# Kernel tuning notes

Measured on AMD Instinct MI355X. Metric: run time of the kernel, lower is better.

## Reference

```python
import jax, jax.numpy as jnp
import numpy as np

N, E, F, H, G = 50000, 1600000, 128, 128, 64
EPS = 1e-5  # BatchNorm eps


def setup_inputs() -> dict:
    key = jax.random.key(0)
    ks = jax.random.split(key, 16)
    x = jax.random.normal(ks[0], (N, F), dtype=jnp.float32)
    edge_index = jax.random.randint(ks[1], (2, E), 0, N, dtype=jnp.int64)
    batch = jnp.sort(jax.random.randint(ks[2], (N,), 0, G, dtype=jnp.int64))
    inp = {
        'x': x, 'edge_index': edge_index, 'batch': batch,
        'W1': jax.random.normal(ks[3], (F, H), dtype=jnp.float32) / np.sqrt(F),
        'b1': jnp.zeros((H,), jnp.float32),
        'bn1_gamma': jax.random.uniform(ks[4], (H,), jnp.float32, 0.5, 1.5),
        'bn1_beta': jax.random.normal(ks[5], (H,), jnp.float32) * 0.1,
        'bn1_mean': jax.random.normal(ks[6], (H,), jnp.float32) * 0.1,
        'bn1_var': jax.random.uniform(ks[7], (H,), jnp.float32, 0.5, 1.5),
        'W2': jax.random.normal(ks[8], (H, H), dtype=jnp.float32) / np.sqrt(H),
        'b2': jnp.zeros((H,), jnp.float32),
        'bn2_gamma': jax.random.uniform(ks[9], (H,), jnp.float32, 0.5, 1.5),
        'bn2_beta': jax.random.normal(ks[10], (H,), jnp.float32) * 0.1,
        'bn2_mean': jax.random.normal(ks[11], (H,), jnp.float32) * 0.1,
        'bn2_var': jax.random.uniform(ks[12], (H,), jnp.float32, 0.5, 1.5),
        'att_w': jax.random.normal(ks[13], (H, 1), dtype=jnp.float32) / np.sqrt(H),
        'cls_w': jax.random.normal(ks[14], (1, H), dtype=jnp.float32) / np.sqrt(H),
        'cls_b': jnp.zeros((1,), jnp.float32),
    }
    return inp


def gcn_conv(h, W, b, src, dst, n):
    # PyG GCNConv: linear, add self-loops, symmetric D^{-1/2}(A+I)D^{-1/2} aggregation, bias.
    hw = h @ W                                   # [n, H]
    loops = jnp.arange(n, dtype=src.dtype)
    s = jnp.concatenate([src, loops])
    d = jnp.concatenate([dst, loops])
    deg = jax.ops.segment_sum(jnp.ones_like(d, dtype=hw.dtype), d, num_segments=n)
    dis = jnp.where(deg > 0, jax.lax.rsqrt(deg), 0.0)
    norm = dis[s] * dis[d]                       # [E+n]
    msgs = hw[s] * norm[:, None]                 # gather + scale (memory-bound)
    return jax.ops.segment_sum(msgs, d, num_segments=n) + b


def batch_norm(h, gamma, beta, mean, var):
    return (h - mean) * gamma * jax.lax.rsqrt(var + EPS) + beta


def reference(x, edge_index, batch, W1, b1, bn1_gamma, bn1_beta, bn1_mean, bn1_var,
              W2, b2, bn2_gamma, bn2_beta, bn2_mean, bn2_var, att_w, cls_w, cls_b):
    n = x.shape[0]
    src, dst = edge_index[0], edge_index[1]
    # eval mode: dropout and edge-dropout are no-ops; BN uses running stats
    h = gcn_conv(x, W1, b1, src, dst, n)
    h = jax.nn.relu(batch_norm(h, bn1_gamma, bn1_beta, bn1_mean, bn1_var))
    h = gcn_conv(h, W2, b2, src, dst, n)
    h = jax.nn.relu(batch_norm(h, bn2_gamma, bn2_beta, bn2_mean, bn2_var))
    att = jax.nn.sigmoid(h @ att_w)              # [n, 1]
    g = jax.ops.segment_sum(h * att, batch, num_segments=G)  # [G, H]
    logits = g @ cls_w.T + cls_b                 # [G, 1]
    return logits, att
```

## Files before the change

### kernel.cpp

```cpp
#include <hip/hip_runtime.h>
#include <math.h>

#define NN 50000
#define HID 128
#define NG 64
#define BN_EPS 1e-5f

typedef __attribute__((ext_vector_type(8))) short short8;
typedef __attribute__((ext_vector_type(4))) float f32x4;

__device__ inline unsigned pack_bf2(float a, float b) {
    union { float f; unsigned u; } ua, ub;
    ua.f = a; ub.f = b;
    unsigned x = ua.u, y = ub.u;
    x += 0x7fffu + ((x >> 16) & 1u);
    y += 0x7fffu + ((y >> 16) & 1u);
    return (x >> 16) | (y & 0xffff0000u);
}
__device__ inline unsigned short bf16_1(float x) {
    union { float f; unsigned u; } v;
    v.f = x;
    unsigned r = v.u + 0x7fffu + ((v.u >> 16) & 1u);
    return (unsigned short)(r >> 16);
}
__device__ inline float2 unpack_bf2(unsigned v) {
    union { unsigned u; float f; } a, b;
    a.u = v << 16;
    b.u = v & 0xffff0000u;
    return make_float2(a.f, b.f);
}

#define NBKT 256
#define ETILE 4096
#define EPT   (ETILE / 256)
#define CAP   10240
#define ASTR 136

__global__ __launch_bounds__(128) void k_prep0(const float* __restrict__ W1,
                                               const float* __restrict__ W2,
                                               unsigned short* __restrict__ wt1,
                                               unsigned short* __restrict__ wt2,
                                               int* __restrict__ bcurP,
                                               const float* __restrict__ cls_b,
                                               float* __restrict__ logits) {
    int b = blockIdx.x;
    int t = threadIdx.x;
    if (b < 256) {
        int k = b & 127;
        const float* W = (b < 128) ? W1 : W2;
        unsigned short* wt = (b < 128) ? wt1 : wt2;
        wt[t * 128 + k] = bf16_1(W[k * 128 + t]);
    } else {
        #pragma unroll
        for (int i = 0; i < 32; ++i) bcurP[t * 32 + i] = 0;
        if (t < NG) logits[t] = cls_b[0];
    }
}

__device__ __forceinline__ void gemm1_tile(char* smem, int row0,
                                           const float* __restrict__ x,
                                           const unsigned short* __restrict__ wt1,
                                           unsigned short* __restrict__ zb,
                                           int n, int t) {
    typedef unsigned short ArowT[ASTR];
    ArowT* A = (ArowT*)smem;
    #pragma unroll
    for (int i = 0; i < 8; ++i) {
        int idx = t + i * 256;
        int r = idx >> 5;
        int c4 = (idx & 31) * 4;
        float4 v = make_float4(0.f, 0.f, 0.f, 0.f);
        if (row0 + r < n) v = *(const float4*)&x[(size_t)(row0 + r) * 128 + c4];
        uint2 p;
        p.x = pack_bf2(v.x, v.y);
        p.y = pack_bf2(v.z, v.w);
        *(uint2*)&A[r][c4] = p;
    }
    __syncthreads();
    int lane = t & 63;
    int wave = t >> 6;
    int m = lane & 15;
    int quad = lane >> 4;
    int r0 = wave * 16;
    short8 a[4];
    #pragma unroll
    for (int kt = 0; kt < 4; ++kt)
        a[kt] = *(const short8*)&A[r0 + m][kt * 32 + quad * 8];
    f32x4 acc[8];
    #pragma unroll
    for (int ct = 0; ct < 8; ++ct) acc[ct] = (f32x4){0.f, 0.f, 0.f, 0.f};
    short8 bcur[4], bnxt[4];
    {
        const unsigned short* wb = &wt1[(size_t)m * 128 + quad * 8];
        #pragma unroll
        for (int kt = 0; kt < 4; ++kt) bcur[kt] = *(const short8*)(wb + kt * 32);
    }
    #pragma unroll
    for (int ct = 0; ct < 8; ++ct) {
        if (ct < 7) {
            const unsigned short* wb = &wt1[(size_t)((ct + 1) * 16 + m) * 128 + quad * 8];
            #pragma unroll
            for (int kt = 0; kt < 4; ++kt) bnxt[kt] = *(const short8*)(wb + kt * 32);
        }
        #pragma unroll
        for (int kt = 0; kt < 4; ++kt)
            acc[ct] = __builtin_amdgcn_mfma_f32_16x16x32_bf16(a[kt], bcur[kt], acc[ct], 0, 0, 0);
        #pragma unroll
        for (int kt = 0; kt < 4; ++kt) bcur[kt] = bnxt[kt];
    }
    __syncthreads();
    #pragma unroll
    for (int ct = 0; ct < 8; ++ct) {
        int col = ct * 16 + m;
        #pragma unroll
        for (int reg = 0; reg < 4; ++reg)
            A[r0 + quad * 4 + reg][col] = bf16_1(acc[ct][reg]);
    }
    __syncthreads();
    #pragma unroll
    for (int i = 0; i < 4; ++i) {
        int idx = t + i * 256;
        int r = idx >> 4;
        int c8 = (idx & 15) * 8;
        int grow = row0 + r;
        if (grow < n)
            *(uint4*)&zb[(size_t)grow * 128 + c8] = *(const uint4*)&A[r][c8];
    }
}

struct SmemDist {
    int h[NBKT], sx[NBKT], cur[NBKT], gb[NBKT];
    unsigned stage[ETILE];
};

__global__ __launch_bounds__(256) void k_dist_gemm1(const int* __restrict__ src,
                                                    const int* __restrict__ dst,
                                                    int* __restrict__ bcurP,
                                                    unsigned* __restrict__ bpacked,
                                                    const float* __restrict__ x,
                                                    const unsigned short* __restrict__ wt1,
                                                    unsigned short* __restrict__ zb,
                                                    int E, int n, int DB) {
    __shared__ __align__(16) char smem[sizeof(SmemDist)];
    int t = threadIdx.x;
    int b = blockIdx.x;

    if (b >= DB) {
        gemm1_tile(smem, (b - DB) * 64, x, wt1, zb, n, t);
        return;
    }
    SmemDist* s = (SmemDist*)smem;
    s->h[t] = 0;
    __syncthreads();
    int base = b * ETILE;
    int dreg[EPT];
    #pragma unroll
    for (int i = 0; i < EPT; ++i) {
        int e = base + i * 256 + t;
        dreg[i] = (e < E) ? dst[e] : -1;
        if (dreg[i] >= 0) atomicAdd(&s->h[dreg[i] >> 8], 1);
    }
    __syncthreads();
    int c = s->h[t];
    s->sx[t] = c;
    __syncthreads();
    for (int off = 1; off < NBKT; off <<= 1) {
        int v = (t >= off) ? s->sx[t - off] : 0;
        __syncthreads();
        s->sx[t] += v;
        __syncthreads();
    }
    int nvalid = s->sx[NBKT - 1];
    int excl = s->sx[t] - c;
    __syncthreads();
    s->sx[t] = excl;
    s->cur[t] = excl;
    s->gb[t] = (c > 0) ? atomicAdd(&bcurP[t * 16], c) : 0;
    __syncthreads();
    #pragma unroll
    for (int i = 0; i < EPT; ++i) {
        int e = base + i * 256 + t;
        if (dreg[i] >= 0) {
            int d = dreg[i];
            int bkt = d >> 8;
            int p = atomicAdd(&s->cur[bkt], 1);
            s->stage[p] = ((unsigned)d << 16) | (unsigned)src[e];
        }
    }
    __syncthreads();
    for (int idx = t; idx < nvalid; idx += 256) {
        unsigned v = s->stage[idx];
        int bkt = (int)(v >> 24);
        int pos = s->gb[bkt] + (idx - s->sx[bkt]);
        bpacked[(size_t)bkt * CAP + pos] = v;
    }
}

struct SmemCSR {
    int cnt[NBKT], sA[NBKT], cur[NBKT];
    unsigned short stage[CAP];
};

__global__ __launch_bounds__(256) void k_csr_gemm1(const unsigned* __restrict__ bpacked,
                                                   const int* __restrict__ bcurP,
                                                   int* __restrict__ row_ptr,
                                                   int* __restrict__ degA,
                                                   float* __restrict__ dis,
                                                   unsigned short* __restrict__ col16,
                                                   const float* __restrict__ x,
                                                   const unsigned short* __restrict__ wt1,
                                                   unsigned short* __restrict__ zb,
                                                   int n, int NB, int row0B) {
    __shared__ __align__(16) char smem[sizeof(SmemCSR)];
    int t = threadIdx.x;
    int b = blockIdx.x;

    if (b >= NB) {
        gemm1_tile(smem, row0B + (b - NB) * 64, x, wt1, zb, n, t);
        return;
    }
    SmemCSR* s = (SmemCSR*)smem;
    int node0 = b << 8;
    int nn = n - node0;
    if (nn > 256) nn = 256;
    if (nn < 0) nn = 0;
    int e0 = b * CAP;
    int ne = bcurP[b * 16];
    s->cnt[t] = 0;
    __syncthreads();
    int n4 = (ne + 3) >> 2;
    for (int i = t; i < n4; i += 256) {
        uint4 v = *(const uint4*)&bpacked[e0 + 4 * i];
        int rem = ne - 4 * i;
        if (rem > 0) atomicAdd(&s->cnt[(v.x >> 16) & 255u], 1);
        if (rem > 1) atomicAdd(&s->cnt[(v.y >> 16) & 255u], 1);
        if (rem > 2) atomicAdd(&s->cnt[(v.z >> 16) & 255u], 1);
        if (rem > 3) atomicAdd(&s->cnt[(v.w >> 16) & 255u], 1);
    }
    __syncthreads();
    int c = s->cnt[t];
    s->sA[t] = c;
    __syncthreads();
    for (int off = 1; off < NBKT; off <<= 1) {
        int v = (t >= off) ? s->sA[t - off] : 0;
        __syncthreads();
        s->sA[t] += v;
        __syncthreads();
    }
    int excl = s->sA[t] - c;
    s->cur[t] = excl;
    if (t < nn) {
        row_ptr[node0 + t] = e0 + excl;
        degA[node0 + t] = c;
        dis[node0 + t] = rsqrtf((float)(c + 1));
    }
    __syncthreads();
    for (int i = t; i < n4; i += 256) {
        uint4 v = *(const uint4*)&bpacked[e0 + 4 * i];
        int rem = ne - 4 * i;
        unsigned vv[4] = {v.x, v.y, v.z, v.w};
        #pragma unroll
        for (int j = 0; j < 4; ++j) {
            if (rem > j) {
                int ld = (int)((vv[j] >> 16) & 255u);
                int p = atomicAdd(&s->cur[ld], 1);
                s->stage[p] = (unsigned short)(vv[j] & 0xFFFFu);
            }
        }
    }
    __syncthreads();
    int nw = (ne + 1) >> 1;
    for (int i = t; i < nw; i += 256) {
        unsigned w = (unsigned)s->stage[2 * i] | ((unsigned)s->stage[2 * i + 1] << 16);
        *(unsigned*)&col16[e0 + 2 * i] = w;
    }
}

__global__ __launch_bounds__(256) void k_scale(unsigned short* __restrict__ zb,
                                               const float* __restrict__ dis, int n) {
    int i = blockIdx.x * 256 + threadIdx.x;
    int r = i >> 4;
    if (r >= n) return;
    int c8 = (i & 15) * 8;
    float s = dis[r];
    uint4 v = *(const uint4*)&zb[(size_t)r * 128 + c8];
    unsigned* w = (unsigned*)&v;
    #pragma unroll
    for (int k = 0; k < 4; ++k) {
        float2 f = unpack_bf2(w[k]);
        w[k] = pack_bf2(f.x * s, f.y * s);
    }
    *(uint4*)&zb[(size_t)r * 128 + c8] = v;
}


__device__ __forceinline__ void gather_pipe(const unsigned short* __restrict__ hws,
                                            const unsigned short* __restrict__ col16,
                                            int e0, int deg, int md, int sl, int part,
                                            float* acc8) {
    int nt = (md + 7) >> 3;
    if (nt <= 0) return;
    int base = part << 4;
    uint4 vA[8], vB[8];
    int c0, c1, n0 = 0, n1 = 0;
    c0 = (sl < deg) ? (int)col16[e0 + sl] : 0;
    c1 = (sl + 16 < deg) ? (int)col16[e0 + 16 + sl] : 0;

    #pragma unroll
    for (int j = 0; j < 8; ++j) {
        int s = __shfl(c0, base + j);
        vA[j] = (j < deg) ? *(const uint4*)(hws + ((size_t)s << 7) + (sl << 3))
                          : make_uint4(0, 0, 0, 0);
    }
    int t = 0, ebase = 0;
    for (;;) {
        if (t + 4 < nt) {
            n0 = (ebase + 32 + sl < deg) ? (int)col16[e0 + ebase + 32 + sl] : 0;
            n1 = (ebase + 48 + sl < deg) ? (int)col16[e0 + ebase + 48 + sl] : 0;
        }
        if (t + 1 < nt) {
            int it0 = (t + 1) << 3;
            #pragma unroll
            for (int j = 0; j < 8; ++j) {
                int s = __shfl(c0, base + 8 + j);
                vB[j] = (it0 + j < deg) ? *(const uint4*)(hws + ((size_t)s << 7) + (sl << 3))
                                        : make_uint4(0, 0, 0, 0);
            }
        }
        #pragma unroll
        for (int j = 0; j < 8; ++j) {
            const unsigned* w = (const unsigned*)&vA[j];
            #pragma unroll
            for (int i2 = 0; i2 < 4; ++i2) {
                float2 f = unpack_bf2(w[i2]);
                acc8[2 * i2]     += f.x;
                acc8[2 * i2 + 1] += f.y;
            }
        }
        if (++t >= nt) break;
        if (t + 1 < nt) {
            int it0 = (t + 1) << 3;
            #pragma unroll
            for (int j = 0; j < 8; ++j) {
                int s = __shfl(c1, base + j);
                vA[j] = (it0 + j < deg) ? *(const uint4*)(hws + ((size_t)s << 7) + (sl << 3))
                                        : make_uint4(0, 0, 0, 0);
            }
        }
        #pragma unroll
        for (int j = 0; j < 8; ++j) {
            const unsigned* w = (const unsigned*)&vB[j];
            #pragma unroll
            for (int i2 = 0; i2 < 4; ++i2) {
                float2 f = unpack_bf2(w[i2]);
                acc8[2 * i2]     += f.x;
                acc8[2 * i2 + 1] += f.y;
            }
        }
        if (++t >= nt) break;
        if (t + 1 < nt) {
            int it0 = (t + 1) << 3;
            #pragma unroll
            for (int j = 0; j < 8; ++j) {
                int s = __shfl(c1, base + 8 + j);
                vB[j] = (it0 + j < deg) ? *(const uint4*)(hws + ((size_t)s << 7) + (sl << 3))
                                        : make_uint4(0, 0, 0, 0);
            }
        }
        #pragma unroll
        for (int j = 0; j < 8; ++j) {
            const unsigned* w = (const unsigned*)&vA[j];
            #pragma unroll
            for (int i2 = 0; i2 < 4; ++i2) {
                float2 f = unpack_bf2(w[i2]);
                acc8[2 * i2]     += f.x;
                acc8[2 * i2 + 1] += f.y;
            }
        }
        if (++t >= nt) break;
        if (t + 1 < nt) {
            int it0 = (t + 1) << 3;
            #pragma unroll
            for (int j = 0; j < 8; ++j) {
                int s = __shfl(n0, base + j);
                vA[j] = (it0 + j < deg) ? *(const uint4*)(hws + ((size_t)s << 7) + (sl << 3))
                                        : make_uint4(0, 0, 0, 0);
            }
        }
        #pragma unroll
        for (int j = 0; j < 8; ++j) {
            const unsigned* w = (const unsigned*)&vB[j];
            #pragma unroll
            for (int i2 = 0; i2 < 4; ++i2) {
                float2 f = unpack_bf2(w[i2]);
                acc8[2 * i2]     += f.x;
                acc8[2 * i2 + 1] += f.y;
            }
        }
        if (++t >= nt) break;
        c0 = n0; c1 = n1; ebase += 32;
    }
}


__global__ __launch_bounds__(256, 3) void k_agg1_gemm2(const unsigned short* __restrict__ zb,
                                                       const int* __restrict__ row_ptr,
                                                       const int* __restrict__ degA,
                                                       const unsigned short* __restrict__ col16,
                                                       const float* __restrict__ dis,
                                                       const float* __restrict__ bias,
                                                       const float* __restrict__ gamma,
                                                       const float* __restrict__ beta,
                                                       const float* __restrict__ mean,
                                                       const float* __restrict__ var,
                                                       const unsigned short* __restrict__ wt2,
                                                       unsigned short* __restrict__ hwsb2, int n) {
    __shared__ unsigned short H1[16][ASTR];
    __shared__ unsigned short C2[16][ASTR];
    int t = threadIdx.x;
    int wave = t >> 6, lane = t & 63;
    int sl = lane & 15, part = lane >> 4;
    int d = blockIdx.x * 16 + wave * 4 + part;
    bool active = (d < n);
    int e0 = 0, deg = 0;
    if (active) {
        e0 = row_ptr[d];
        deg = degA[d];
    }
    uint4 vs = make_uint4(0, 0, 0, 0);
    float dd = 0.f;
    if (active) {
        vs = *(const uint4*)(zb + ((size_t)d << 7) + (sl << 3));
        dd = dis[d];
    }
    int md = deg;
    md = max(md, __shfl_xor(md, 16));
    md = max(md, __shfl_xor(md, 32));

    float acc8[8] = {0, 0, 0, 0, 0, 0, 0, 0};
    gather_pipe(zb, col16, e0, deg, md, sl, part, acc8);

    unsigned outw[4] = {0, 0, 0, 0};
    if (active) {
        const unsigned* w = (const unsigned*)&vs;
        #pragma unroll
        for (int i2 = 0; i2 < 4; ++i2) {
            float2 f = unpack_bf2(w[i2]);
            acc8[2 * i2]     += f.x;
            acc8[2 * i2 + 1] += f.y;
        }
        int f0 = sl << 3;
        #pragma unroll
        for (int i2 = 0; i2 < 4; ++i2) {
            int f = f0 + 2 * i2;
            float2 bv = *(const float2*)&bias[f];
            float2 gm = *(const float2*)&gamma[f];
            float2 bt = *(const float2*)&beta[f];
            float2 mn = *(const float2*)&mean[f];
            float2 vr = *(const float2*)&var[f];
            float vx = acc8[2 * i2] * dd + bv.x;
            float vy = acc8[2 * i2 + 1] * dd + bv.y;
            float sx = gm.x * rsqrtf(vr.x + BN_EPS);
            float sy = gm.y * rsqrtf(vr.y + BN_EPS);
            float rx = fmaxf((vx - mn.x) * sx + bt.x, 0.f);
            float ry = fmaxf((vy - mn.y) * sy + bt.y, 0.f);
            outw[i2] = pack_bf2(rx, ry);
        }
    }
    int local = wave * 4 + part;
    *(uint4*)&H1[local][sl << 3] = *(uint4*)outw;
    __syncthreads();

    int m = sl;
    int quad = part;
    short8 a2[4];
    #pragma unroll
    for (int kt = 0; kt < 4; ++kt)
        a2[kt] = *(const short8*)&H1[m][kt * 32 + quad * 8];

    f32x4 acc2[2];
    acc2[0] = (f32x4){0.f, 0.f, 0.f, 0.f};
    acc2[1] = (f32x4){0.f, 0.f, 0.f, 0.f};
    #pragma unroll
    for (int i = 0; i < 2; ++i) {
        int ct = wave * 2 + i;
        const unsigned short* wb = &wt2[(size_t)(ct * 16 + m) * 128 + quad * 8];
        #pragma unroll
        for (int kt = 0; kt < 4; ++kt) {
            short8 b = *(const short8*)(wb + kt * 32);
            acc2[i] = __builtin_amdgcn_mfma_f32_16x16x32_bf16(a2[kt], b, acc2[i], 0, 0, 0);
        }
    }
    int gr = blockIdx.x * 16 + quad * 4;
    float ds2[4];
    #pragma unroll
    for (int reg = 0; reg < 4; ++reg)
        ds2[reg] = (gr + reg < n) ? dis[gr + reg] : 0.f;
    #pragma unroll
    for (int i = 0; i < 2; ++i) {
        int col = (wave * 2 + i) * 16 + m;
        #pragma unroll
        for (int reg = 0; reg < 4; ++reg)
            C2[quad * 4 + reg][col] = bf16_1(acc2[i][reg] * ds2[reg]);
    }
    __syncthreads();
    {
        int r = t >> 4;
        int c8 = (t & 15) * 8;
        int grow = blockIdx.x * 16 + r;
        if (grow < n)
            *(uint4*)&hwsb2[(size_t)grow * 128 + c8] = *(const uint4*)&C2[r][c8];
    }
}


__global__ __launch_bounds__(256, 3) void k_agg2_att_logit(const unsigned short* __restrict__ hwsb,
                                                           const int* __restrict__ row_ptr,
                                                           const int* __restrict__ degA,
                                                           const unsigned short* __restrict__ col16,
                                                           const float* __restrict__ dis,
                                                           const float* __restrict__ bias,
                                                           const float* __restrict__ gamma,
                                                           const float* __restrict__ beta,
                                                           const float* __restrict__ mean,
                                                           const float* __restrict__ var,
                                                           const int* __restrict__ batch,
                                                           const float* __restrict__ att_w,
                                                           const float* __restrict__ cls_w,
                                                           float* __restrict__ att_out,
                                                           float* __restrict__ logits, int n) {
    __shared__ int   sg[16];
    __shared__ float sv[16];
    int t = threadIdx.x;
    int wave = t >> 6, lane = t & 63;
    int sl = lane & 15, part = lane >> 4;
    int d = blockIdx.x * 16 + wave * 4 + part;
    bool active = (d < n);
    int e0 = 0, deg = 0;
    if (active) {
        e0 = row_ptr[d];
        deg = degA[d];
    }
    uint4 vs = make_uint4(0, 0, 0, 0);
    float dd = 0.f;
    int g = -1;
    if (active) {
        vs = *(const uint4*)(hwsb + ((size_t)d << 7) + (sl << 3));
        dd = dis[d];
        g = batch[d];
    }
    int md = deg;
    md = max(md, __shfl_xor(md, 16));
    md = max(md, __shfl_xor(md, 32));

    float acc8[8] = {0, 0, 0, 0, 0, 0, 0, 0};
    gather_pipe(hwsb, col16, e0, deg, md, sl, part, acc8);

    float contrib = 0.f;
    float p = 0.f, q = 0.f;
    if (active) {
        const unsigned* w = (const unsigned*)&vs;
        #pragma unroll
        for (int i2 = 0; i2 < 4; ++i2) {
            float2 f = unpack_bf2(w[i2]);
            acc8[2 * i2]     += f.x;
            acc8[2 * i2 + 1] += f.y;
        }
        int f0 = sl << 3;
        #pragma unroll
        for (int i2 = 0; i2 < 4; ++i2) {
            int f = f0 + 2 * i2;
            float2 bv = *(const float2*)&bias[f];
            float2 gm = *(const float2*)&gamma[f];
            float2 bt = *(const float2*)&beta[f];
            float2 mn = *(const float2*)&mean[f];
            float2 vr = *(const float2*)&var[f];
            float vx = acc8[2 * i2] * dd + bv.x;
            float vy = acc8[2 * i2 + 1] * dd + bv.y;
            float sx = gm.x * rsqrtf(vr.x + BN_EPS);
            float sy = gm.y * rsqrtf(vr.y + BN_EPS);
            float rx = fmaxf((vx - mn.x) * sx + bt.x, 0.f);
            float ry = fmaxf((vy - mn.y) * sy + bt.y, 0.f);
            float2 aw = *(const float2*)&att_w[f];
            float2 cw = *(const float2*)&cls_w[f];
            p += rx * aw.x + ry * aw.y;
            q += rx * cw.x + ry * cw.y;
        }
    }
    #pragma unroll
    for (int off = 1; off < 16; off <<= 1) {
        p += __shfl_xor(p, off);
        q += __shfl_xor(q, off);
    }
    if (active) {
        float a = 1.f / (1.f + expf(-p));
        if (sl == 0) att_out[d] = a;
        contrib = a * q;
    }
    if (sl == 0) {
        sg[wave * 4 + part] = g;
        sv[wave * 4 + part] = contrib;
    }
    __syncthreads();
    if (t == 0) {
        int cur = -1;
        float acc = 0.f;
        #pragma unroll
        for (int i = 0; i < 16; ++i) {
            int gi = sg[i];
            if (gi < 0) continue;
            if (gi != cur) {
                if (cur >= 0) atomicAdd(&logits[cur], acc);
                cur = gi;
                acc = 0.f;
            }
            acc += sv[i];
        }
        if (cur >= 0) atomicAdd(&logits[cur], acc);
    }
}


extern "C" void kernel_launch(void* const* d_in, const int* in_sizes, int n_in,
                              void* d_out, int out_size, void* d_ws, size_t ws_size,
                              hipStream_t stream) {
    const float* x   = (const float*)d_in[0];
    const int*   ei  = (const int*)d_in[1];
    const int*   bat = (const int*)d_in[2];
    const float* W1  = (const float*)d_in[3];
    const float* b1  = (const float*)d_in[4];
    const float* g1  = (const float*)d_in[5];
    const float* bt1 = (const float*)d_in[6];
    const float* mn1 = (const float*)d_in[7];
    const float* vr1 = (const float*)d_in[8];
    const float* W2  = (const float*)d_in[9];
    const float* b2  = (const float*)d_in[10];
    const float* g2  = (const float*)d_in[11];
    const float* bt2 = (const float*)d_in[12];
    const float* mn2 = (const float*)d_in[13];
    const float* vr2 = (const float*)d_in[14];
    const float* attw = (const float*)d_in[15];
    const float* clsw = (const float*)d_in[16];
    const float* clsb = (const float*)d_in[17];

    int E = in_sizes[1] / 2;
    int n = in_sizes[2];
    const int* src = ei;
    const int* dst = ei + E;
    int NB = (n + 255) >> 8;

    char* ws = (char*)d_ws;
    auto alloc = [&](size_t bytes) {
        void* p = (void*)ws;
        ws += (bytes + 255) & ~(size_t)255;
        return p;
    };
    int*            bcurP   = (int*)alloc(NBKT * 16 * 4);
    unsigned*       bpacked = (unsigned*)alloc((size_t)NBKT * CAP * 4);
    int*            row_ptr = (int*)alloc((size_t)n * 4);
    int*            degA    = (int*)alloc((size_t)n * 4);
    unsigned short* col16   = (unsigned short*)alloc(((size_t)NBKT * CAP + 1024) * 2);
    float*          dis     = (float*)alloc((size_t)n * 4);
    unsigned short* zb      = (unsigned short*)alloc((size_t)n * 128 * 2);
    unsigned short* hwsb2   = (unsigned short*)alloc((size_t)n * 128 * 2);
    unsigned short* wt1     = (unsigned short*)alloc(128 * 128 * 2);
    unsigned short* wt2     = (unsigned short*)alloc(128 * 128 * 2);

    float* out = (float*)d_out;
    int DB = (E + ETILE - 1) / ETILE;
    int gb = (n + 63) / 64;
    int G1A = gb / 2;
    int G1B = gb - G1A;
    int ab = (n + 15) / 16;
    int sb = (n * 16 + 255) / 256;

    k_prep0<<<257, 128, 0, stream>>>(W1, W2, wt1, wt2, bcurP, clsb, out);
    k_dist_gemm1<<<DB + G1A, 256, 0, stream>>>(src, dst, bcurP, bpacked, x, wt1, zb,
                                               E, n, DB);
    k_csr_gemm1<<<NB + G1B, 256, 0, stream>>>(bpacked, bcurP, row_ptr, degA, dis,
                                              col16, x, wt1, zb, n, NB, G1A * 64);
    k_scale<<<sb, 256, 0, stream>>>(zb, dis, n);
    k_agg1_gemm2<<<ab, 256, 0, stream>>>(zb, row_ptr, degA, col16, dis,
                                         b1, g1, bt1, mn1, vr1, wt2, hwsb2, n);
    k_agg2_att_logit<<<ab, 256, 0, stream>>>(hwsb2, row_ptr, degA, col16, dis,
                                             b2, g2, bt2, mn2, vr2, bat, attw, clsw,
                                             out + NG, out, n);
}
```

Before: 265.1 us.

## Replace atomic bucket distribution with histogram-scan-scatter and fuse scaling into CSR

```diff
diff --git a/kernel.cpp b/kernel.cpp
--- a/kernel.cpp
+++ b/kernel.cpp
@@ -40,7 +40,6 @@
                                                const float* __restrict__ W2,
                                                unsigned short* __restrict__ wt1,
                                                unsigned short* __restrict__ wt2,
-                                               int* __restrict__ bcurP,
                                                const float* __restrict__ cls_b,
                                                float* __restrict__ logits) {
     int b = blockIdx.x;
@@ -51,8 +50,6 @@
         unsigned short* wt = (b < 128) ? wt1 : wt2;
         wt[t * 128 + k] = bf16_1(W[k * 128 + t]);
     } else {
-        #pragma unroll
-        for (int i = 0; i < 32; ++i) bcurP[t * 32 + i] = 0;
         if (t < NG) logits[t] = cls_b[0];
     }
 }
@@ -128,28 +125,85 @@
     }
 }
 
+__global__ __launch_bounds__(256) void k_hist_gemm1(const int* __restrict__ dst,
+                                                    int* __restrict__ hist,
+                                                    const float* __restrict__ x,
+                                                    const unsigned short* __restrict__ wt1,
+                                                    unsigned short* __restrict__ zb,
+                                                    int E, int n, int DB) {
+    __shared__ __align__(16) char smem[64 * ASTR * 2];
+    int t = threadIdx.x;
+    int b = blockIdx.x;
+    if (b >= DB) {
+        gemm1_tile(smem, (b - DB) * 64, x, wt1, zb, n, t);
+        return;
+    }
+    int* h = (int*)smem;
+    h[t] = 0;
+    __syncthreads();
+    int base = b * ETILE;
+    #pragma unroll
+    for (int i = 0; i < EPT; ++i) {
+        int e = base + i * 256 + t;
+        if (e < E) atomicAdd(&h[dst[e] >> 8], 1);
+    }
+    __syncthreads();
+    hist[t * DB + b] = h[t];
+}
+
+__global__ __launch_bounds__(256) void k_scan(const int* __restrict__ hist,
+                                              int* __restrict__ off,
+                                              int* __restrict__ bcurP, int DB) {
+    __shared__ int sc[512];
+    int k = blockIdx.x, t = threadIdx.x;
+    int v0 = (t < DB) ? hist[k * DB + t] : 0;
+    int v1 = (256 + t < DB) ? hist[k * DB + 256 + t] : 0;
+    sc[t] = v0;
+    sc[256 + t] = v1;
+    __syncthreads();
+    for (int o = 1; o < 256; o <<= 1) {
+        int a = (t >= o) ? sc[t - o] : 0;
+        __syncthreads();
+        sc[t] += a;
+        __syncthreads();
+    }
+    for (int o = 1; o < 256; o <<= 1) {
+        int a = (t >= o) ? sc[256 + t - o] : 0;
+        __syncthreads();
+        sc[256 + t] += a;
+        __syncthreads();
+    }
+    int add = sc[255];
+    sc[256 + t] += add;
+    __syncthreads();
+    int base = k * CAP;
+    if (t < DB) off[k * DB + t] = base + sc[t] - v0;
+    if (256 + t < DB) off[k * DB + 256 + t] = base + sc[256 + t] - v1;
+    if (t == 0) bcurP[k * 16] = sc[511];
+}
+
 struct SmemDist {
     int h[NBKT], sx[NBKT], cur[NBKT], gb[NBKT];
     unsigned stage[ETILE];
 };
 
-__global__ __launch_bounds__(256) void k_dist_gemm1(const int* __restrict__ src,
-                                                    const int* __restrict__ dst,
-                                                    int* __restrict__ bcurP,
-                                                    unsigned* __restrict__ bpacked,
-                                                    const float* __restrict__ x,
-                                                    const unsigned short* __restrict__ wt1,
-                                                    unsigned short* __restrict__ zb,
-                                                    int E, int n, int DB) {
+__global__ __launch_bounds__(256) void k_scatter_gemm1(const int* __restrict__ src,
+                                                       const int* __restrict__ dst,
+                                                       const int* __restrict__ off,
+                                                       unsigned* __restrict__ bpacked,
+                                                       const float* __restrict__ x,
+                                                       const unsigned short* __restrict__ wt1,
+                                                       unsigned short* __restrict__ zb,
+                                                       int E, int n, int DB, int row0B) {
     __shared__ __align__(16) char smem[sizeof(SmemDist)];
     int t = threadIdx.x;
     int b = blockIdx.x;
-
     if (b >= DB) {
-        gemm1_tile(smem, (b - DB) * 64, x, wt1, zb, n, t);
+        gemm1_tile(smem, row0B + (b - DB) * 64, x, wt1, zb, n, t);
         return;
     }
     SmemDist* s = (SmemDist*)smem;
+    int mygb = off[t * DB + b];
     s->h[t] = 0;
     __syncthreads();
     int base = b * ETILE;
@@ -164,8 +218,8 @@
     int c = s->h[t];
     s->sx[t] = c;
     __syncthreads();
-    for (int off = 1; off < NBKT; off <<= 1) {
-        int v = (t >= off) ? s->sx[t - off] : 0;
+    for (int o = 1; o < NBKT; o <<= 1) {
+        int v = (t >= o) ? s->sx[t - o] : 0;
         __syncthreads();
         s->sx[t] += v;
         __syncthreads();
@@ -175,7 +229,7 @@
     __syncthreads();
     s->sx[t] = excl;
     s->cur[t] = excl;
-    s->gb[t] = (c > 0) ? atomicAdd(&bcurP[t * 16], c) : 0;
+    s->gb[t] = mygb;
     __syncthreads();
     #pragma unroll
     for (int i = 0; i < EPT; ++i) {
@@ -191,35 +245,28 @@
     for (int idx = t; idx < nvalid; idx += 256) {
         unsigned v = s->stage[idx];
         int bkt = (int)(v >> 24);
-        int pos = s->gb[bkt] + (idx - s->sx[bkt]);
-        bpacked[(size_t)bkt * CAP + pos] = v;
+        bpacked[s->gb[bkt] + (idx - s->sx[bkt])] = v;
     }
 }
 
 struct SmemCSR {
     int cnt[NBKT], sA[NBKT], cur[NBKT];
+    float disL[NBKT];
     unsigned short stage[CAP];
 };
 
-__global__ __launch_bounds__(256) void k_csr_gemm1(const unsigned* __restrict__ bpacked,
+__global__ __launch_bounds__(256) void k_csr_scale(const unsigned* __restrict__ bpacked,
                                                    const int* __restrict__ bcurP,
                                                    int* __restrict__ row_ptr,
                                                    int* __restrict__ degA,
                                                    float* __restrict__ dis,
                                                    unsigned short* __restrict__ col16,
-                                                   const float* __restrict__ x,
-                                                   const unsigned short* __restrict__ wt1,
                                                    unsigned short* __restrict__ zb,
-                                                   int n, int NB, int row0B) {
-    __shared__ __align__(16) char smem[sizeof(SmemCSR)];
+                                                   int n) {
+    __shared__ __align__(16) char smemc[sizeof(SmemCSR)];
+    SmemCSR* s = (SmemCSR*)smemc;
     int t = threadIdx.x;
     int b = blockIdx.x;
-
-    if (b >= NB) {
-        gemm1_tile(smem, row0B + (b - NB) * 64, x, wt1, zb, n, t);
-        return;
-    }
-    SmemCSR* s = (SmemCSR*)smem;
     int node0 = b << 8;
     int nn = n - node0;
     if (nn > 256) nn = 256;
@@ -241,18 +288,20 @@
     int c = s->cnt[t];
     s->sA[t] = c;
     __syncthreads();
-    for (int off = 1; off < NBKT; off <<= 1) {
-        int v = (t >= off) ? s->sA[t - off] : 0;
+    for (int o = 1; o < NBKT; o <<= 1) {
+        int v = (t >= o) ? s->sA[t - o] : 0;
         __syncthreads();
         s->sA[t] += v;
         __syncthreads();
     }
     int excl = s->sA[t] - c;
     s->cur[t] = excl;
+    float dv = rsqrtf((float)(c + 1));
+    s->disL[t] = dv;
     if (t < nn) {
         row_ptr[node0 + t] = e0 + excl;
         degA[node0 + t] = c;
-        dis[node0 + t] = rsqrtf((float)(c + 1));
+        dis[node0 + t] = dv;
     }
     __syncthreads();
     for (int i = t; i < n4; i += 256) {
@@ -274,23 +323,20 @@
         unsigned w = (unsigned)s->stage[2 * i] | ((unsigned)s->stage[2 * i + 1] << 16);
         *(unsigned*)&col16[e0 + 2 * i] = w;
     }
-}
-
-__global__ __launch_bounds__(256) void k_scale(unsigned short* __restrict__ zb,
-                                               const float* __restrict__ dis, int n) {
-    int i = blockIdx.x * 256 + threadIdx.x;
-    int r = i >> 4;
-    if (r >= n) return;
-    int c8 = (i & 15) * 8;
-    float s = dis[r];
-    uint4 v = *(const uint4*)&zb[(size_t)r * 128 + c8];
-    unsigned* w = (unsigned*)&v;
-    #pragma unroll
-    for (int k = 0; k < 4; ++k) {
-        float2 f = unpack_bf2(w[k]);
-        w[k] = pack_bf2(f.x * s, f.y * s);
-    }
-    *(uint4*)&zb[(size_t)r * 128 + c8] = v;
+    for (int idx = t; idx < nn * 16; idx += 256) {
+        int r = idx >> 4;
+        int c8 = (idx & 15) * 8;
+        float sc = s->disL[r];
+        size_t o8 = (size_t)(node0 + r) * 128 + c8;
+        uint4 v = *(const uint4*)&zb[o8];
+        unsigned* w = (unsigned*)&v;
+        #pragma unroll
+        for (int k2 = 0; k2 < 4; ++k2) {
+            float2 f = unpack_bf2(w[k2]);
+            w[k2] = pack_bf2(f.x * sc, f.y * sc);
+        }
+        *(uint4*)&zb[o8] = v;
+    }
 }
 
 
@@ -655,6 +701,8 @@
         ws += (bytes + 255) & ~(size_t)255;
         return p;
     };
+    int DB = (E + ETILE - 1) / ETILE;
+
     int*            bcurP   = (int*)alloc(NBKT * 16 * 4);
     unsigned*       bpacked = (unsigned*)alloc((size_t)NBKT * CAP * 4);
     int*            row_ptr = (int*)alloc((size_t)n * 4);
@@ -665,21 +713,22 @@
     unsigned short* hwsb2   = (unsigned short*)alloc((size_t)n * 128 * 2);
     unsigned short* wt1     = (unsigned short*)alloc(128 * 128 * 2);
     unsigned short* wt2     = (unsigned short*)alloc(128 * 128 * 2);
+    int*            hist    = (int*)alloc((size_t)NBKT * DB * 4);
+    int*            offs    = (int*)alloc((size_t)NBKT * DB * 4);
 
     float* out = (float*)d_out;
-    int DB = (E + ETILE - 1) / ETILE;
     int gb = (n + 63) / 64;
     int G1A = gb / 2;
     int G1B = gb - G1A;
     int ab = (n + 15) / 16;
-    int sb = (n * 16 + 255) / 256;
-
-    k_prep0<<<257, 128, 0, stream>>>(W1, W2, wt1, wt2, bcurP, clsb, out);
-    k_dist_gemm1<<<DB + G1A, 256, 0, stream>>>(src, dst, bcurP, bpacked, x, wt1, zb,
-                                               E, n, DB);
-    k_csr_gemm1<<<NB + G1B, 256, 0, stream>>>(bpacked, bcurP, row_ptr, degA, dis,
-                                              col16, x, wt1, zb, n, NB, G1A * 64);
-    k_scale<<<sb, 256, 0, stream>>>(zb, dis, n);
+
+    k_prep0<<<257, 128, 0, stream>>>(W1, W2, wt1, wt2, clsb, out);
+    k_hist_gemm1<<<DB + G1A, 256, 0, stream>>>(dst, hist, x, wt1, zb, E, n, DB);
+    k_scan<<<NBKT, 256, 0, stream>>>(hist, offs, bcurP, DB);
+    k_scatter_gemm1<<<DB + G1B, 256, 0, stream>>>(src, dst, offs, bpacked, x, wt1, zb,
+                                                  E, n, DB, G1A * 64);
+    k_csr_scale<<<NB, 256, 0, stream>>>(bpacked, bcurP, row_ptr, degA, dis,
+                                        col16, zb, n);
     k_agg1_gemm2<<<ab, 256, 0, stream>>>(zb, row_ptr, degA, col16, dis,
                                          b1, g1, bt1, mn1, vr1, wt2, hwsb2, n);
     k_agg2_att_logit<<<ab, 256, 0, stream>>>(hwsb2, row_ptr, degA, col16, dis,
```

After: 272.9 us. 1.03x slower.
